# Kernel optimization log

Hardware: AMD Instinct MI355X
Metric: run time of the kernel (lower is better)

## Reference

```python
import jax, jax.numpy as jnp
from jax import lax
import numpy as np

B, T = 8, 65536
IN_CH, OUT_CH = 1, 2
RES_CH, SKIP_CH = 32, 64
KS, DEPTH, STACKS = 3, 8, 2
L = DEPTH * STACKS
DILATIONS = [2 ** (i % DEPTH) for i in range(L)]


def causal_conv1d(x, w, b, dilation=1):
    # x: (B, Cin, T), w: (Cout, Cin, K) -> (B, Cout, T), left-padded causal
    pad = (w.shape[-1] - 1) * dilation
    out = lax.conv_general_dilated(
        x, w, window_strides=(1,), padding=[(pad, 0)],
        rhs_dilation=(dilation,), dimension_numbers=('NCH', 'OIH', 'NCH'))
    return out + b[None, :, None]


def setup_inputs() -> dict:
    key = jax.random.key(0)
    ks = jax.random.split(key, 16)
    s = 0.05  # small init keeps exp(0.5*log_var) well-behaved
    inp = {
        'x': jax.random.normal(ks[0], (B, IN_CH, T), jnp.float32),
        'W_in': jax.random.normal(ks[1], (L, RES_CH, IN_CH, 1), jnp.float32) * s,
        'b_in': jnp.zeros((L, RES_CH), jnp.float32),
        'W_f': jax.random.normal(ks[2], (L, RES_CH, RES_CH, KS), jnp.float32) * s,
        'b_f': jnp.zeros((L, RES_CH), jnp.float32),
        'W_g': jax.random.normal(ks[3], (L, RES_CH, RES_CH, KS), jnp.float32) * s,
        'b_g': jnp.zeros((L, RES_CH), jnp.float32),
        'W_s': jax.random.normal(ks[4], (L, SKIP_CH, RES_CH, 1), jnp.float32) * s,
        'b_s': jnp.zeros((L, SKIP_CH), jnp.float32),
        'W_o': jax.random.normal(ks[5], (L, IN_CH, RES_CH, 1), jnp.float32) * s,
        'b_o': jnp.zeros((L, IN_CH), jnp.float32),
        'W_sk1': jax.random.normal(ks[6], (SKIP_CH, SKIP_CH, 1), jnp.float32) * s,
        'b_sk1': jnp.zeros((SKIP_CH,), jnp.float32),
        'W_sk2': jax.random.normal(ks[7], (OUT_CH, SKIP_CH, 1), jnp.float32) * s,
        'b_sk2': jnp.zeros((OUT_CH,), jnp.float32),
    }
    return inp


def reference(x, W_in, b_in, W_f, b_f, W_g, b_g, W_s, b_s, W_o, b_o,
              W_sk1, b_sk1, W_sk2, b_sk2):
    out = x
    skip_acc = jnp.zeros((x.shape[0], SKIP_CH, x.shape[2]), x.dtype)
    for i in range(L):
        d = DILATIONS[i]
        residual = causal_conv1d(out, W_in[i], b_in[i])           # (B,res,T)
        f = jnp.tanh(causal_conv1d(residual, W_f[i], b_f[i], d))
        g = jax.nn.sigmoid(causal_conv1d(residual, W_g[i], b_g[i], d))
        gated = f * g
        skip_acc = skip_acc + causal_conv1d(gated, W_s[i], b_s[i])
        out = causal_conv1d(gated, W_o[i], b_o[i]) + out
    skip = jax.nn.relu(causal_conv1d(skip_acc, W_sk1, b_sk1))
    output = causal_conv1d(skip, W_sk2, b_sk2)                    # (B,2,T)
    means = output[:, 0, :]
    stds = jnp.exp(0.5 * output[:, 1, :])
    return means, stds
```

## Files before the change

kernel.cpp:

```cpp
#include <hip/hip_runtime.h>
#include <hip/hip_bf16.h>
#include <math.h>

#define T_LEN 65536
#define B_N   8
#define BT    (T_LEN * B_N)
#define L_N   16
#define RC    32
#define SC    64

#define NT1   256
#define CL    512

#define TS    128

#define A_AF0 0
#define A_AF1 32
#define A_AF2 64
#define A_CF0 96
#define A_CF1 128
#define A_BFC 160
#define A_AG0 192
#define A_AG1 224
#define A_AG2 256
#define A_CG0 288
#define A_CG1 320
#define A_BGC 352
#define A_BFI 384
#define A_BGI 416
#define FW_L  448
#define FW_BSUM (L_N * FW_L)
#define FW_F32  (FW_BSUM + 64)
#define WSBF_N  (L_N * SC * RC)
#define W1BF_N  (SC * SC)

typedef float v2f __attribute__((ext_vector_type(2)));
typedef __attribute__((ext_vector_type(4))) float f4;
typedef __attribute__((ext_vector_type(8))) short bf8;

#define MFMA16(a, b, c) __builtin_amdgcn_mfma_f32_16x16x32_bf16(a, b, c, 0, 0, 0)

__device__ __forceinline__ float fast_rcp(float x) { return __builtin_amdgcn_rcpf(x); }

__device__ __forceinline__ float gated_fn(float fp, float gp) {
    float E = __builtin_amdgcn_exp2f(fp);
    float F = __builtin_amdgcn_exp2f(gp);
    return (E - 1.f) * F * fast_rcp((E + 1.f) * (F + 1.f));
}

__device__ __forceinline__ unsigned short f2bf(float f) {
    unsigned u = __float_as_uint(f);
    u += 0x7fffu + ((u >> 16) & 1u);
    return (unsigned short)(u >> 16);
}

__device__ __forceinline__ unsigned pk2(float lo, float hi) {
    __hip_bfloat162 h = __float22bfloat162_rn(make_float2(lo, hi));
    unsigned u; __builtin_memcpy(&u, &h, 4); return u;
}

__device__ __forceinline__ bf8 mk_bf8(unsigned a, unsigned b, unsigned c, unsigned d) {
    unsigned v[4] = {a, b, c, d};
    bf8 r; __builtin_memcpy(&r, v, 16); return r;
}

__global__ __launch_bounds__(256) void prep_kernel(
    const float* __restrict__ W_f, const float* __restrict__ W_g,
    const float* __restrict__ W_in, const float* __restrict__ b_in,
    const float* __restrict__ b_f, const float* __restrict__ b_g,
    const float* __restrict__ b_s, const float* __restrict__ W_s,
    const float* __restrict__ W_sk1, float* __restrict__ fw,
    short* __restrict__ fwh)
{
    const float SF = 2.88539008177792681472f;
    const float SG = 1.44269504088896340736f;
    int idx = blockIdx.x * 256 + threadIdx.x;
    if (idx < L_N * RC) {
        int i = idx >> 5, c = idx & 31;
        float af[3] = {0,0,0}, cf[3] = {0,0,0}, ag[3] = {0,0,0}, cg[3] = {0,0,0};
        for (int cin = 0; cin < RC; ++cin) {
            float wi = W_in[i * RC + cin];
            float bi = b_in[i * RC + cin];
            #pragma unroll
            for (int k = 0; k < 3; ++k) {
                float wf = W_f[((i * RC + c) * RC + cin) * 3 + k];
                float wg = W_g[((i * RC + c) * RC + cin) * 3 + k];
                af[k] = fmaf(wf, wi, af[k]);
                cf[k] = fmaf(wf, bi, cf[k]);
                ag[k] = fmaf(wg, wi, ag[k]);
                cg[k] = fmaf(wg, bi, cg[k]);
            }
        }
        float* p = fw + i * FW_L;
        p[A_AF0 + c] = af[0] * SF; p[A_AF1 + c] = af[1] * SF; p[A_AF2 + c] = af[2] * SF;
        p[A_CF0 + c] = cf[0] * SF; p[A_CF1 + c] = cf[1] * SF;
        p[A_BFC + c] = (b_f[i * RC + c] + cf[2]) * SF;
        p[A_BFI + c] = (b_f[i * RC + c] + cf[2] + cf[0] + cf[1]) * SF;
        p[A_AG0 + c] = ag[0] * SG; p[A_AG1 + c] = ag[1] * SG; p[A_AG2 + c] = ag[2] * SG;
        p[A_CG0 + c] = cg[0] * SG; p[A_CG1 + c] = cg[1] * SG;
        p[A_BGC + c] = (b_g[i * RC + c] + cg[2]) * SG;
        p[A_BGI + c] = (b_g[i * RC + c] + cg[2] + cg[0] + cg[1]) * SG;
    } else if (idx < L_N * RC + SC) {
        int s = idx - L_N * RC;
        float acc = 0.f;
        for (int i = 0; i < L_N; ++i) acc += b_s[i * SC + s];
        fw[FW_BSUM + s] = acc;
    } else if (idx < 576 + WSBF_N) {
        int j = idx - 576;
        fwh[j] = (short)f2bf(W_s[j]);
    } else if (idx < 576 + WSBF_N + W1BF_N) {
        int j = idx - 576 - WSBF_N;
        fwh[WSBF_N + j] = (short)f2bf(W_sk1[j]);
    }
}

__global__ __launch_bounds__(NT1) void layer_kernel(
    const float* __restrict__ src, float* __restrict__ dst,
    const float* __restrict__ gwl, const float* __restrict__ wol,
    const float* __restrict__ bol, int d)
{
    int b     = blockIdx.x >> 7;
    int chunk = blockIdx.x & 127;
    int t0    = chunk * CL;
    const float* sb = src + (size_t)b * T_LEN;
    float*       db = dst + (size_t)b * T_LEN;
    int tid = threadIdx.x;
    int h   = 2 * d;

    int ta = t0 + tid, tb = ta + NT1;
    v2f s2p, s1p, s0p;
    v2f accp = (v2f){0.f, 0.f};

    if (chunk != 0) {
        s2p.x = sb[ta];     s2p.y = sb[tb];
        s1p.x = sb[ta - d]; s1p.y = sb[tb - d];
        s0p.x = sb[ta - h]; s0p.y = sb[tb - h];
        for (int c4 = 0; c4 < 8; ++c4) {
            f4 vaf0 = *(const f4*)(gwl + A_AF0 + c4 * 4);
            f4 vaf1 = *(const f4*)(gwl + A_AF1 + c4 * 4);
            f4 vaf2 = *(const f4*)(gwl + A_AF2 + c4 * 4);
            f4 vbfi = *(const f4*)(gwl + A_BFI + c4 * 4);
            f4 vag0 = *(const f4*)(gwl + A_AG0 + c4 * 4);
            f4 vag1 = *(const f4*)(gwl + A_AG1 + c4 * 4);
            f4 vag2 = *(const f4*)(gwl + A_AG2 + c4 * 4);
            f4 vbgi = *(const f4*)(gwl + A_BGI + c4 * 4);
            f4 vwo  = *(const f4*)(wol + c4 * 4);
            #pragma unroll
            for (int e = 0; e < 4; ++e) {
                float af0 = vaf0[e], af1 = vaf1[e], af2 = vaf2[e], bfi = vbfi[e];
                float ag0 = vag0[e], ag1 = vag1[e], ag2 = vag2[e], bgi = vbgi[e];
                float woc = vwo[e];
                v2f fp = (v2f){bfi, bfi} + s0p * (v2f){af0, af0} + s1p * (v2f){af1, af1} + s2p * (v2f){af2, af2};
                v2f gp = (v2f){bgi, bgi} + s0p * (v2f){ag0, ag0} + s1p * (v2f){ag1, ag1} + s2p * (v2f){ag2, ag2};
                v2f g;
                g.x = gated_fn(fp.x, gp.x);
                g.y = gated_fn(fp.y, gp.y);
                accp = accp + g * (v2f){woc, woc};
            }
        }
    } else {
        v2f m1p, m0p;
        m1p.x = (ta >= d) ? 1.f : 0.f; m1p.y = (tb >= d) ? 1.f : 0.f;
        m0p.x = (ta >= h) ? 1.f : 0.f; m0p.y = (tb >= h) ? 1.f : 0.f;
        s2p.x = sb[ta];
        s2p.y = sb[tb];
        s1p.x = (ta >= d) ? sb[ta - d] : 0.f;
        s1p.y = (tb >= d) ? sb[tb - d] : 0.f;
        s0p.x = (ta >= h) ? sb[ta - h] : 0.f;
        s0p.y = (tb >= h) ? sb[tb - h] : 0.f;
        for (int c4 = 0; c4 < 8; ++c4) {
            f4 vaf0 = *(const f4*)(gwl + A_AF0 + c4 * 4);
            f4 vaf1 = *(const f4*)(gwl + A_AF1 + c4 * 4);
            f4 vaf2 = *(const f4*)(gwl + A_AF2 + c4 * 4);
            f4 vcf0 = *(const f4*)(gwl + A_CF0 + c4 * 4);
            f4 vcf1 = *(const f4*)(gwl + A_CF1 + c4 * 4);
            f4 vbfc = *(const f4*)(gwl + A_BFC + c4 * 4);
            f4 vag0 = *(const f4*)(gwl + A_AG0 + c4 * 4);
            f4 vag1 = *(const f4*)(gwl + A_AG1 + c4 * 4);
            f4 vag2 = *(const f4*)(gwl + A_AG2 + c4 * 4);
            f4 vcg0 = *(const f4*)(gwl + A_CG0 + c4 * 4);
            f4 vcg1 = *(const f4*)(gwl + A_CG1 + c4 * 4);
            f4 vbgc = *(const f4*)(gwl + A_BGC + c4 * 4);
            f4 vwo  = *(const f4*)(wol + c4 * 4);
            #pragma unroll
            for (int e = 0; e < 4; ++e) {
                float af0 = vaf0[e], af1 = vaf1[e], af2 = vaf2[e];
                float cf0 = vcf0[e], cf1 = vcf1[e], bfc = vbfc[e];
                float ag0 = vag0[e], ag1 = vag1[e], ag2 = vag2[e];
                float cg0 = vcg0[e], cg1 = vcg1[e], bgc = vbgc[e];
                float woc = vwo[e];
                v2f fp = (v2f){bfc, bfc} + m0p * (v2f){cf0, cf0} + m1p * (v2f){cf1, cf1};
                fp = fp + s0p * (v2f){af0, af0} + s1p * (v2f){af1, af1} + s2p * (v2f){af2, af2};
                v2f gp = (v2f){bgc, bgc} + m0p * (v2f){cg0, cg0} + m1p * (v2f){cg1, cg1};
                gp = gp + s0p * (v2f){ag0, ag0} + s1p * (v2f){ag1, ag1} + s2p * (v2f){ag2, ag2};
                v2f g;
                g.x = gated_fn(fp.x, gp.x);
                g.y = gated_fn(fp.y, gp.y);
                accp = accp + g * (v2f){woc, woc};
            }
        }
    }
    float bo = *bol;
    db[ta] = s2p.x + bo + accp.x;
    db[tb] = s2p.y + bo + accp.y;
}

#define SMB_W    0
#define SMB_MISC 28672
#define SMB_TOT  29712

__global__ __launch_bounds__(256) void pass2_kernel(
    const float* __restrict__ x, const float* __restrict__ streams,
    const float* __restrict__ fw, const short* __restrict__ Wsbf,
    const short* __restrict__ W1bf, const float* __restrict__ b_sk1,
    const float* __restrict__ W_sk2, const float* __restrict__ b_sk2,
    float* __restrict__ out)
{
    __shared__ __align__(16) char smb[SMB_TOT];
    float* sW    = (float*)smb;
    float* sMisc = (float*)(smb + SMB_MISC);

    int tid   = threadIdx.x;
    int b     = blockIdx.x >> 9;
    int chunk = blockIdx.x & 511;
    int t0    = chunk * TS;

    for (int j = tid; j < (L_N * FW_L) / 4; j += 256)
        ((f4*)sW)[j] = ((const f4*)fw)[j];
    if (tid < 64) { sMisc[tid] = fw[FW_BSUM + tid]; sMisc[64 + tid] = b_sk1[tid]; }
    if (tid < 128) sMisc[128 + tid] = W_sk2[tid];
    if (tid < 2)   sMisc[256 + tid] = b_sk2[tid];
    __syncthreads();

    int wv   = tid >> 6;
    int lane = tid & 63;
    int m    = lane & 15;
    int q    = lane >> 4;

    int tr0 = t0 + wv * 32 + m;
    int tr1 = tr0 + 16;

    f4 zero4 = {0.f, 0.f, 0.f, 0.f};
    f4 acc[2][4];
    #pragma unroll
    for (int tt = 0; tt < 2; ++tt)
        #pragma unroll
        for (int st = 0; st < 4; ++st) acc[tt][st] = zero4;

    const float* xb = x + (size_t)b * T_LEN;
    #pragma unroll
    for (int i = 0; i < L_N; ++i) {
        const int d = 1 << (i & 7);
        const float* src = (i == 0) ? xb
                                    : (streams + (size_t)(i - 1) * BT + (size_t)b * T_LEN);
        const float* w = sW + i * FW_L + q * 8;

        bf8 bfrag[4];
        #pragma unroll
        for (int st = 0; st < 4; ++st)
            bfrag[st] = *(const bf8*)(Wsbf + i * (SC * RC) + (st * 16 + m) * RC + q * 8);

        unsigned uf[2][4];
        if (t0 >= 2 * d) {
            float s2a = src[tr0], s1a = src[tr0 - d], s0a = src[tr0 - 2 * d];
            float s2b = src[tr1], s1b = src[tr1 - d], s0b = src[tr1 - 2 * d];
            #pragma unroll
            for (int hc = 0; hc < 2; ++hc) {
                const float* wc = w + hc * 4;
                f4 af0 = *(const f4*)(wc + A_AF0), af1 = *(const f4*)(wc + A_AF1), af2 = *(const f4*)(wc + A_AF2);
                f4 bfi = *(const f4*)(wc + A_BFI);
                f4 ag0 = *(const f4*)(wc + A_AG0), ag1 = *(const f4*)(wc + A_AG1), ag2 = *(const f4*)(wc + A_AG2);
                f4 bgi = *(const f4*)(wc + A_BGI);
                f4 fpa = bfi + s0a * af0 + s1a * af1 + s2a * af2;
                f4 gpa = bgi + s0a * ag0 + s1a * ag1 + s2a * ag2;
                f4 fpb = bfi + s0b * af0 + s1b * af1 + s2b * af2;
                f4 gpb = bgi + s0b * ag0 + s1b * ag1 + s2b * ag2;
                uf[0][hc * 2 + 0] = pk2(gated_fn(fpa[0], gpa[0]), gated_fn(fpa[1], gpa[1]));
                uf[0][hc * 2 + 1] = pk2(gated_fn(fpa[2], gpa[2]), gated_fn(fpa[3], gpa[3]));
                uf[1][hc * 2 + 0] = pk2(gated_fn(fpb[0], gpb[0]), gated_fn(fpb[1], gpb[1]));
                uf[1][hc * 2 + 1] = pk2(gated_fn(fpb[2], gpb[2]), gated_fn(fpb[3], gpb[3]));
            }
        } else {
            float m1a = (tr0 >= d) ? 1.f : 0.f, m0a = (tr0 >= 2 * d) ? 1.f : 0.f;
            float m1b = (tr1 >= d) ? 1.f : 0.f, m0b = (tr1 >= 2 * d) ? 1.f : 0.f;
            float s2a = src[tr0];
            float s1a = (tr0 >= d)     ? src[tr0 - d]     : 0.f;
            float s0a = (tr0 >= 2 * d) ? src[tr0 - 2 * d] : 0.f;
            float s2b = src[tr1];
            float s1b = (tr1 >= d)     ? src[tr1 - d]     : 0.f;
            float s0b = (tr1 >= 2 * d) ? src[tr1 - 2 * d] : 0.f;
            #pragma unroll
            for (int hc = 0; hc < 2; ++hc) {
                const float* wc = w + hc * 4;
                f4 af0 = *(const f4*)(wc + A_AF0), af1 = *(const f4*)(wc + A_AF1), af2 = *(const f4*)(wc + A_AF2);
                f4 cf0 = *(const f4*)(wc + A_CF0), cf1 = *(const f4*)(wc + A_CF1), bfc = *(const f4*)(wc + A_BFC);
                f4 ag0 = *(const f4*)(wc + A_AG0), ag1 = *(const f4*)(wc + A_AG1), ag2 = *(const f4*)(wc + A_AG2);
                f4 cg0 = *(const f4*)(wc + A_CG0), cg1 = *(const f4*)(wc + A_CG1), bgc = *(const f4*)(wc + A_BGC);
                f4 fpa = bfc + m0a * cf0 + m1a * cf1 + s0a * af0 + s1a * af1 + s2a * af2;
                f4 gpa = bgc + m0a * cg0 + m1a * cg1 + s0a * ag0 + s1a * ag1 + s2a * ag2;
                f4 fpb = bfc + m0b * cf0 + m1b * cf1 + s0b * af0 + s1b * af1 + s2b * af2;
                f4 gpb = bgc + m0b * cg0 + m1b * cg1 + s0b * ag0 + s1b * ag1 + s2b * ag2;
                uf[0][hc * 2 + 0] = pk2(gated_fn(fpa[0], gpa[0]), gated_fn(fpa[1], gpa[1]));
                uf[0][hc * 2 + 1] = pk2(gated_fn(fpa[2], gpa[2]), gated_fn(fpa[3], gpa[3]));
                uf[1][hc * 2 + 0] = pk2(gated_fn(fpb[0], gpb[0]), gated_fn(fpb[1], gpb[1]));
                uf[1][hc * 2 + 1] = pk2(gated_fn(fpb[2], gpb[2]), gated_fn(fpb[3], gpb[3]));
            }
        }

        bf8 a0 = mk_bf8(uf[0][0], uf[0][1], uf[0][2], uf[0][3]);
        bf8 a1 = mk_bf8(uf[1][0], uf[1][1], uf[1][2], uf[1][3]);
        #pragma unroll
        for (int st = 0; st < 4; ++st) {
            acc[0][st] = MFMA16(a0, bfrag[st], acc[0][st]);
            acc[1][st] = MFMA16(a1, bfrag[st], acc[1][st]);
        }
    }

    __syncthreads();
    #pragma unroll
    for (int tt = 0; tt < 2; ++tt) {
        int tb = (wv * 2 + tt) * 16 + q * 4;
        #pragma unroll
        for (int st = 0; st < 4; ++st) {
            int s = st * 16 + m;
            float bs = sMisc[s];
            #pragma unroll
            for (int r = 0; r < 4; ++r)
                *(unsigned short*)(smb + (tb + r) * 144 + s * 2) = f2bf(acc[tt][st][r] + bs);
        }
    }
    bf8 w1f[4][2];
    #pragma unroll
    for (int ot = 0; ot < 4; ++ot)
        #pragma unroll
        for (int kc = 0; kc < 2; ++kc)
            w1f[ot][kc] = *(const bf8*)(W1bf + (ot * 16 + m) * SC + kc * 32 + q * 8);
    __syncthreads();

    f4 hacc[2][4];
    #pragma unroll
    for (int tt = 0; tt < 2; ++tt)
        #pragma unroll
        for (int ot = 0; ot < 4; ++ot) hacc[tt][ot] = zero4;
    #pragma unroll
    for (int tt = 0; tt < 2; ++tt) {
        int trow = (wv * 2 + tt) * 16 + m;
        #pragma unroll
        for (int kc = 0; kc < 2; ++kc) {
            bf8 afrag = *(const bf8*)(smb + trow * 144 + kc * 64 + q * 16);
            #pragma unroll
            for (int ot = 0; ot < 4; ++ot)
                hacc[tt][ot] = MFMA16(afrag, w1f[ot][kc], hacc[tt][ot]);
        }
    }

    float p0[2][4], p1[2][4];
    #pragma unroll
    for (int tt = 0; tt < 2; ++tt)
        #pragma unroll
        for (int r = 0; r < 4; ++r) { p0[tt][r] = 0.f; p1[tt][r] = 0.f; }
    #pragma unroll
    for (int ot = 0; ot < 4; ++ot) {
        int o = ot * 16 + m;
        float w20 = sMisc[128 + o], w21 = sMisc[192 + o], b1v = sMisc[64 + o];
        #pragma unroll
        for (int tt = 0; tt < 2; ++tt)
            #pragma unroll
            for (int r = 0; r < 4; ++r) {
                float hv = fmaxf(hacc[tt][ot][r] + b1v, 0.f);
                p0[tt][r] = fmaf(w20, hv, p0[tt][r]);
                p1[tt][r] = fmaf(w21, hv, p1[tt][r]);
            }
    }
    #pragma unroll
    for (int msk = 1; msk <= 8; msk <<= 1) {
        #pragma unroll
        for (int tt = 0; tt < 2; ++tt)
            #pragma unroll
            for (int r = 0; r < 4; ++r) {
                p0[tt][r] += __shfl_xor(p0[tt][r], msk);
                p1[tt][r] += __shfl_xor(p1[tt][r], msk);
            }
    }
    if (m == 0) {
        float b20 = sMisc[256], b21 = sMisc[257];
        #pragma unroll
        for (int tt = 0; tt < 2; ++tt) {
            int t = t0 + (wv * 2 + tt) * 16 + q * 4;
            size_t gi = (size_t)b * T_LEN + t;
            f4 mv, sv;
            #pragma unroll
            for (int r = 0; r < 4; ++r) {
                mv[r] = p0[tt][r] + b20;
                sv[r] = __expf(0.5f * (p1[tt][r] + b21));
            }
            *(f4*)(out + gi)      = mv;
            *(f4*)(out + BT + gi) = sv;
        }
    }
}

extern "C" void kernel_launch(void* const* d_in, const int* in_sizes, int n_in,
                              void* d_out, int out_size, void* d_ws, size_t ws_size,
                              hipStream_t stream) {
    const float* x     = (const float*)d_in[0];
    const float* W_in  = (const float*)d_in[1];
    const float* b_in  = (const float*)d_in[2];
    const float* W_f   = (const float*)d_in[3];
    const float* b_f   = (const float*)d_in[4];
    const float* W_g   = (const float*)d_in[5];
    const float* b_g   = (const float*)d_in[6];
    const float* W_s   = (const float*)d_in[7];
    const float* b_s   = (const float*)d_in[8];
    const float* W_o   = (const float*)d_in[9];
    const float* b_o   = (const float*)d_in[10];
    const float* W_sk1 = (const float*)d_in[11];
    const float* b_sk1 = (const float*)d_in[12];
    const float* W_sk2 = (const float*)d_in[13];
    const float* b_sk2 = (const float*)d_in[14];
    float* outp = (float*)d_out;

    float* streams = (float*)d_ws;
    float* fw      = streams + (size_t)15 * BT;
    short* fwh     = (short*)(fw + FW_F32);

    int prep_items = 576 + WSBF_N + W1BF_N;
    prep_kernel<<<(prep_items + 255) / 256, 256, 0, stream>>>(
        W_f, W_g, W_in, b_in, b_f, b_g, b_s, W_s, W_sk1, fw, fwh);
    for (int i = 0; i < 15; ++i) {
        int d = 1 << (i & 7);
        const float* src = (i == 0) ? x : streams + (size_t)(i - 1) * BT;
        layer_kernel<<<B_N * (T_LEN / CL), NT1, 0, stream>>>(
            src, streams + (size_t)i * BT, fw + i * FW_L, W_o + i * 32, b_o + i, d);
    }
    pass2_kernel<<<B_N * (T_LEN / TS), 256, 0, stream>>>(
        x, streams, fw, fwh, fwh + WSBF_N, b_sk1, W_sk2, b_sk2, outp);
}
```

Before: 431.8 us.

## Cache gated activations in bf16 from layer kernels for reuse in pass2

Layer kernels now also write the 32-channel gated activations as bf16 to workspace buffers, when the workspace has room. Pass2 then loads these directly as MFMA A-fragments instead of recomputing the dilated convolutions and tanh/sigmoid per layer. This trades transcendental recompute in pass2 for a large extra memory write and read: about 32 MB per layer, up to 15 layers. Whether the path runs depends on ws_size, and the extra memory traffic may outweigh the saved compute.

```diff
diff --git a/kernel.cpp b/kernel.cpp
--- a/kernel.cpp
+++ b/kernel.cpp
@@ -117,7 +117,7 @@
 __global__ __launch_bounds__(NT1) void layer_kernel(
     const float* __restrict__ src, float* __restrict__ dst,
     const float* __restrict__ gwl, const float* __restrict__ wol,
-    const float* __restrict__ bol, int d)
+    const float* __restrict__ bol, int d, short* __restrict__ Gout)
 {
     int b     = blockIdx.x >> 7;
     int chunk = blockIdx.x & 127;
@@ -130,6 +130,13 @@
     int ta = t0 + tid, tb = ta + NT1;
     v2f s2p, s1p, s0p;
     v2f accp = (v2f){0.f, 0.f};
+
+    short* Ga  = nullptr;
+    short* Gb2 = nullptr;
+    if (Gout) {
+        Ga  = Gout + ((size_t)b * T_LEN + ta) * 32;
+        Gb2 = Ga + (size_t)NT1 * 32;
+    }
 
     if (chunk != 0) {
         s2p.x = sb[ta];     s2p.y = sb[tb];
@@ -145,6 +152,7 @@
             f4 vag2 = *(const f4*)(gwl + A_AG2 + c4 * 4);
             f4 vbgi = *(const f4*)(gwl + A_BGI + c4 * 4);
             f4 vwo  = *(const f4*)(wol + c4 * 4);
+            float gax[4], gbx[4];
             #pragma unroll
             for (int e = 0; e < 4; ++e) {
                 float af0 = vaf0[e], af1 = vaf1[e], af2 = vaf2[e], bfi = vbfi[e];
@@ -156,6 +164,11 @@
                 g.x = gated_fn(fp.x, gp.x);
                 g.y = gated_fn(fp.y, gp.y);
                 accp = accp + g * (v2f){woc, woc};
+                gax[e] = g.x; gbx[e] = g.y;
+            }
+            if (Gout) {
+                *(uint2*)(Ga  + c4 * 4) = make_uint2(pk2(gax[0], gax[1]), pk2(gax[2], gax[3]));
+                *(uint2*)(Gb2 + c4 * 4) = make_uint2(pk2(gbx[0], gbx[1]), pk2(gbx[2], gbx[3]));
             }
         }
     } else {
@@ -182,6 +195,7 @@
             f4 vcg1 = *(const f4*)(gwl + A_CG1 + c4 * 4);
             f4 vbgc = *(const f4*)(gwl + A_BGC + c4 * 4);
             f4 vwo  = *(const f4*)(wol + c4 * 4);
+            float gax[4], gbx[4];
             #pragma unroll
             for (int e = 0; e < 4; ++e) {
                 float af0 = vaf0[e], af1 = vaf1[e], af2 = vaf2[e];
@@ -197,6 +211,11 @@
                 g.x = gated_fn(fp.x, gp.x);
                 g.y = gated_fn(fp.y, gp.y);
                 accp = accp + g * (v2f){woc, woc};
+                gax[e] = g.x; gbx[e] = g.y;
+            }
+            if (Gout) {
+                *(uint2*)(Ga  + c4 * 4) = make_uint2(pk2(gax[0], gax[1]), pk2(gax[2], gax[3]));
+                *(uint2*)(Gb2 + c4 * 4) = make_uint2(pk2(gbx[0], gbx[1]), pk2(gbx[2], gbx[3]));
             }
         }
     }
@@ -214,7 +233,7 @@
     const float* __restrict__ fw, const short* __restrict__ Wsbf,
     const short* __restrict__ W1bf, const float* __restrict__ b_sk1,
     const float* __restrict__ W_sk2, const float* __restrict__ b_sk2,
-    float* __restrict__ out)
+    const short* __restrict__ G, int nG, float* __restrict__ out)
 {
     __shared__ __align__(16) char smb[SMB_TOT];
     float* sW    = (float*)smb;
@@ -248,67 +267,73 @@
         for (int st = 0; st < 4; ++st) acc[tt][st] = zero4;
 
     const float* xb = x + (size_t)b * T_LEN;
-    #pragma unroll
     for (int i = 0; i < L_N; ++i) {
         const int d = 1 << (i & 7);
-        const float* src = (i == 0) ? xb
-                                    : (streams + (size_t)(i - 1) * BT + (size_t)b * T_LEN);
-        const float* w = sW + i * FW_L + q * 8;
 
         bf8 bfrag[4];
         #pragma unroll
         for (int st = 0; st < 4; ++st)
             bfrag[st] = *(const bf8*)(Wsbf + i * (SC * RC) + (st * 16 + m) * RC + q * 8);
 
-        unsigned uf[2][4];
-        if (t0 >= 2 * d) {
-            float s2a = src[tr0], s1a = src[tr0 - d], s0a = src[tr0 - 2 * d];
-            float s2b = src[tr1], s1b = src[tr1 - d], s0b = src[tr1 - 2 * d];
-            #pragma unroll
-            for (int hc = 0; hc < 2; ++hc) {
-                const float* wc = w + hc * 4;
-                f4 af0 = *(const f4*)(wc + A_AF0), af1 = *(const f4*)(wc + A_AF1), af2 = *(const f4*)(wc + A_AF2);
-                f4 bfi = *(const f4*)(wc + A_BFI);
-                f4 ag0 = *(const f4*)(wc + A_AG0), ag1 = *(const f4*)(wc + A_AG1), ag2 = *(const f4*)(wc + A_AG2);
-                f4 bgi = *(const f4*)(wc + A_BGI);
-                f4 fpa = bfi + s0a * af0 + s1a * af1 + s2a * af2;
-                f4 gpa = bgi + s0a * ag0 + s1a * ag1 + s2a * ag2;
-                f4 fpb = bfi + s0b * af0 + s1b * af1 + s2b * af2;
-                f4 gpb = bgi + s0b * ag0 + s1b * ag1 + s2b * ag2;
-                uf[0][hc * 2 + 0] = pk2(gated_fn(fpa[0], gpa[0]), gated_fn(fpa[1], gpa[1]));
-                uf[0][hc * 2 + 1] = pk2(gated_fn(fpa[2], gpa[2]), gated_fn(fpa[3], gpa[3]));
-                uf[1][hc * 2 + 0] = pk2(gated_fn(fpb[0], gpb[0]), gated_fn(fpb[1], gpb[1]));
-                uf[1][hc * 2 + 1] = pk2(gated_fn(fpb[2], gpb[2]), gated_fn(fpb[3], gpb[3]));
-            }
+        bf8 a0, a1;
+        if (i < nG) {
+            const short* Gl = G + (size_t)i * BT * 32 + (size_t)b * T_LEN * 32;
+            a0 = *(const bf8*)(Gl + (size_t)tr0 * 32 + q * 8);
+            a1 = *(const bf8*)(Gl + (size_t)tr1 * 32 + q * 8);
         } else {
-            float m1a = (tr0 >= d) ? 1.f : 0.f, m0a = (tr0 >= 2 * d) ? 1.f : 0.f;
-            float m1b = (tr1 >= d) ? 1.f : 0.f, m0b = (tr1 >= 2 * d) ? 1.f : 0.f;
-            float s2a = src[tr0];
-            float s1a = (tr0 >= d)     ? src[tr0 - d]     : 0.f;
-            float s0a = (tr0 >= 2 * d) ? src[tr0 - 2 * d] : 0.f;
-            float s2b = src[tr1];
-            float s1b = (tr1 >= d)     ? src[tr1 - d]     : 0.f;
-            float s0b = (tr1 >= 2 * d) ? src[tr1 - 2 * d] : 0.f;
-            #pragma unroll
-            for (int hc = 0; hc < 2; ++hc) {
-                const float* wc = w + hc * 4;
-                f4 af0 = *(const f4*)(wc + A_AF0), af1 = *(const f4*)(wc + A_AF1), af2 = *(const f4*)(wc + A_AF2);
-                f4 cf0 = *(const f4*)(wc + A_CF0), cf1 = *(const f4*)(wc + A_CF1), bfc = *(const f4*)(wc + A_BFC);
-                f4 ag0 = *(const f4*)(wc + A_AG0), ag1 = *(const f4*)(wc + A_AG1), ag2 = *(const f4*)(wc + A_AG2);
-                f4 cg0 = *(const f4*)(wc + A_CG0), cg1 = *(const f4*)(wc + A_CG1), bgc = *(const f4*)(wc + A_BGC);
-                f4 fpa = bfc + m0a * cf0 + m1a * cf1 + s0a * af0 + s1a * af1 + s2a * af2;
-                f4 gpa = bgc + m0a * cg0 + m1a * cg1 + s0a * ag0 + s1a * ag1 + s2a * ag2;
-                f4 fpb = bfc + m0b * cf0 + m1b * cf1 + s0b * af0 + s1b * af1 + s2b * af2;
-                f4 gpb = bgc + m0b * cg0 + m1b * cg1 + s0b * ag0 + s1b * ag1 + s2b * ag2;
-                uf[0][hc * 2 + 0] = pk2(gated_fn(fpa[0], gpa[0]), gated_fn(fpa[1], gpa[1]));
-                uf[0][hc * 2 + 1] = pk2(gated_fn(fpa[2], gpa[2]), gated_fn(fpa[3], gpa[3]));
-                uf[1][hc * 2 + 0] = pk2(gated_fn(fpb[0], gpb[0]), gated_fn(fpb[1], gpb[1]));
-                uf[1][hc * 2 + 1] = pk2(gated_fn(fpb[2], gpb[2]), gated_fn(fpb[3], gpb[3]));
-            }
-        }
-
-        bf8 a0 = mk_bf8(uf[0][0], uf[0][1], uf[0][2], uf[0][3]);
-        bf8 a1 = mk_bf8(uf[1][0], uf[1][1], uf[1][2], uf[1][3]);
+            const float* src = (i == 0) ? xb
+                                        : (streams + (size_t)(i - 1) * BT + (size_t)b * T_LEN);
+            const float* w = sW + i * FW_L + q * 8;
+            unsigned uf[2][4];
+            if (t0 >= 2 * d) {
+                float s2a = src[tr0], s1a = src[tr0 - d], s0a = src[tr0 - 2 * d];
+                float s2b = src[tr1], s1b = src[tr1 - d], s0b = src[tr1 - 2 * d];
+                #pragma unroll
+                for (int hc = 0; hc < 2; ++hc) {
+                    const float* wc = w + hc * 4;
+                    f4 af0 = *(const f4*)(wc + A_AF0), af1 = *(const f4*)(wc + A_AF1), af2 = *(const f4*)(wc + A_AF2);
+                    f4 bfi = *(const f4*)(wc + A_BFI);
+                    f4 ag0 = *(const f4*)(wc + A_AG0), ag1 = *(const f4*)(wc + A_AG1), ag2 = *(const f4*)(wc + A_AG2);
+                    f4 bgi = *(const f4*)(wc + A_BGI);
+                    f4 fpa = bfi + s0a * af0 + s1a * af1 + s2a * af2;
+                    f4 gpa = bgi + s0a * ag0 + s1a * ag1 + s2a * ag2;
+                    f4 fpb = bfi + s0b * af0 + s1b * af1 + s2b * af2;
+                    f4 gpb = bgi + s0b * ag0 + s1b * ag1 + s2b * ag2;
+                    uf[0][hc * 2 + 0] = pk2(gated_fn(fpa[0], gpa[0]), gated_fn(fpa[1], gpa[1]));
+                    uf[0][hc * 2 + 1] = pk2(gated_fn(fpa[2], gpa[2]), gated_fn(fpa[3], gpa[3]));
+                    uf[1][hc * 2 + 0] = pk2(gated_fn(fpb[0], gpb[0]), gated_fn(fpb[1], gpb[1]));
+                    uf[1][hc * 2 + 1] = pk2(gated_fn(fpb[2], gpb[2]), gated_fn(fpb[3], gpb[3]));
+                }
+            } else {
+                float m1a = (tr0 >= d) ? 1.f : 0.f, m0a = (tr0 >= 2 * d) ? 1.f : 0.f;
+                float m1b = (tr1 >= d) ? 1.f : 0.f, m0b = (tr1 >= 2 * d) ? 1.f : 0.f;
+                float s2a = src[tr0];
+                float s1a = (tr0 >= d)     ? src[tr0 - d]     : 0.f;
+                float s0a = (tr0 >= 2 * d) ? src[tr0 - 2 * d] : 0.f;
+                float s2b = src[tr1];
+                float s1b = (tr1 >= d)     ? src[tr1 - d]     : 0.f;
+                float s0b = (tr1 >= 2 * d) ? src[tr1 - 2 * d] : 0.f;
+                #pragma unroll
+                for (int hc = 0; hc < 2; ++hc) {
+                    const float* wc = w + hc * 4;
+                    f4 af0 = *(const f4*)(wc + A_AF0), af1 = *(const f4*)(wc + A_AF1), af2 = *(const f4*)(wc + A_AF2);
+                    f4 cf0 = *(const f4*)(wc + A_CF0), cf1 = *(const f4*)(wc + A_CF1), bfc = *(const f4*)(wc + A_BFC);
+                    f4 ag0 = *(const f4*)(wc + A_AG0), ag1 = *(const f4*)(wc + A_AG1), ag2 = *(const f4*)(wc + A_AG2);
+                    f4 cg0 = *(const f4*)(wc + A_CG0), cg1 = *(const f4*)(wc + A_CG1), bgc = *(const f4*)(wc + A_BGC);
+                    f4 fpa = bfc + m0a * cf0 + m1a * cf1 + s0a * af0 + s1a * af1 + s2a * af2;
+                    f4 gpa = bgc + m0a * cg0 + m1a * cg1 + s0a * ag0 + s1a * ag1 + s2a * ag2;
+                    f4 fpb = bfc + m0b * cf0 + m1b * cf1 + s0b * af0 + s1b * af1 + s2b * af2;
+                    f4 gpb = bgc + m0b * cg0 + m1b * cg1 + s0b * ag0 + s1b * ag1 + s2b * ag2;
+                    uf[0][hc * 2 + 0] = pk2(gated_fn(fpa[0], gpa[0]), gated_fn(fpa[1], gpa[1]));
+                    uf[0][hc * 2 + 1] = pk2(gated_fn(fpa[2], gpa[2]), gated_fn(fpa[3], gpa[3]));
+                    uf[1][hc * 2 + 0] = pk2(gated_fn(fpb[0], gpb[0]), gated_fn(fpb[1], gpb[1]));
+                    uf[1][hc * 2 + 1] = pk2(gated_fn(fpb[2], gpb[2]), gated_fn(fpb[3], gpb[3]));
+                }
+            }
+            a0 = mk_bf8(uf[0][0], uf[0][1], uf[0][2], uf[0][3]);
+            a1 = mk_bf8(uf[1][0], uf[1][1], uf[1][2], uf[1][3]);
+        }
+
         #pragma unroll
         for (int st = 0; st < 4; ++st) {
             acc[0][st] = MFMA16(a0, bfrag[st], acc[0][st]);
@@ -423,6 +448,16 @@
     float* streams = (float*)d_ws;
     float* fw      = streams + (size_t)15 * BT;
     short* fwh     = (short*)(fw + FW_F32);
+    short* G       = fwh + WSBF_N + W1BF_N;
+
+    size_t base = (size_t)15 * BT * 4 + (size_t)FW_F32 * 4
+                + (size_t)(WSBF_N + W1BF_N) * 2;
+    size_t perG = (size_t)BT * RC * 2;
+    int nG = 0;
+    if (ws_size > base) {
+        size_t fit = (ws_size - base) / perG;
+        nG = (fit > 15) ? 15 : (int)fit;
+    }
 
     int prep_items = 576 + WSBF_N + W1BF_N;
     prep_kernel<<<(prep_items + 255) / 256, 256, 0, stream>>>(
@@ -430,9 +465,10 @@
     for (int i = 0; i < 15; ++i) {
         int d = 1 << (i & 7);
         const float* src = (i == 0) ? x : streams + (size_t)(i - 1) * BT;
+        short* Gout = (i < nG) ? (G + (size_t)i * BT * RC) : nullptr;
         layer_kernel<<<B_N * (T_LEN / CL), NT1, 0, stream>>>(
-            src, streams + (size_t)i * BT, fw + i * FW_L, W_o + i * 32, b_o + i, d);
+            src, streams + (size_t)i * BT, fw + i * FW_L, W_o + i * 32, b_o + i, d, Gout);
     }
     pass2_kernel<<<B_N * (T_LEN / TS), 256, 0, stream>>>(
-        x, streams, fw, fwh, fwh + WSBF_N, b_sk1, W_sk2, b_sk2, outp);
-}
+        x, streams, fw, fwh, fwh + WSBF_N, b_sk1, W_sk2, b_sk2, G, nG, outp);
+}
```

Measured after the change: 503.5 us. 1.17x slower.
